# Kernel tuning notes

Measured on AMD Instinct MI355X. Metric: run time of the kernel, lower is better.

## Reference

```python
import jax, jax.numpy as jnp
import numpy as np

N_NODES = 50000
N_EDGES = 800000
IN_DIM = 256
OUT_DIM = 64
NEG_SLOPE = 0.01  # torch F.leaky_relu default


def setup_inputs() -> dict:
    key = jax.random.key(0)
    k1, k2, k3, k4, k5 = jax.random.split(key, 5)
    return {
        "h": jax.random.normal(k1, (N_NODES, IN_DIM), dtype=jnp.float32),
        "src": jax.random.randint(k2, (N_EDGES,), 0, N_NODES, dtype=jnp.int32),
        "dst": jax.random.randint(k3, (N_EDGES,), 0, N_NODES, dtype=jnp.int32),
        "W_fc": jax.random.normal(k4, (IN_DIM, OUT_DIM), dtype=jnp.float32) / np.sqrt(IN_DIM),
        "a_vec": jax.random.normal(k5, (2 * OUT_DIM,), dtype=jnp.float32) / np.sqrt(2 * OUT_DIM),
    }


def reference(h, src, dst, W_fc, a_vec):
    n = h.shape[0]
    d = W_fc.shape[1]
    # z = fc(h)
    z = h @ W_fc  # [N, out_dim]
    # edge attention: attn_fc(cat[z_src, z_dst]) == z_src@a[:d] + z_dst@a[d:]
    s_src = z @ a_vec[:d]  # [N]
    s_dst = z @ a_vec[d:]  # [N]
    e = jax.nn.leaky_relu(s_src[src] + s_dst[dst], negative_slope=NEG_SLOPE)  # [E]
    # segment softmax over incoming edges of each dst node (stable)
    e_max = jax.ops.segment_max(e, dst, num_segments=n)  # -inf for isolated nodes (unused)
    e_exp = jnp.exp(e - e_max[dst])
    denom = jax.ops.segment_sum(e_exp, dst, num_segments=n)
    alpha = e_exp / denom[dst]  # [E]
    # weighted scatter-sum of source features
    out = jax.ops.segment_sum(alpha[:, None] * z[src], dst, num_segments=n)  # [N, out_dim]
    return out
```

## Files before the change

kernel.cpp:

```cpp
#include <hip/hip_runtime.h>

#define IN_DIM 256
#define OUT_DIM 64
#define NEG_SLOPE 0.01f
#define SCAN_CHUNK 2048

__global__ __launch_bounds__(256) void gemm_z(const float* __restrict__ h,
                                              const float* __restrict__ W,
                                              const float* __restrict__ a,
                                              float* __restrict__ z,
                                              float* __restrict__ s_src,
                                              float* __restrict__ s_dst, int n) {
    __shared__ float hT[64][68];
    __shared__ float Wc[64][OUT_DIM];
    const int tid = threadIdx.x;
    const int row0 = blockIdx.x * 64;
    const int tr = tid >> 4;
    const int tc = tid & 15;

    float acc[4][4] = {};

    for (int kc = 0; kc < IN_DIM / 64; ++kc) {
        __syncthreads();
        #pragma unroll
        for (int p = 0; p < 4; ++p) {
            int r  = (tid >> 4) + p * 16;
            int k4 = (tid & 15) * 4;
            int grow = row0 + r;
            float4 hv = make_float4(0.f, 0.f, 0.f, 0.f);
            if (grow < n)
                hv = *(const float4*)&h[(size_t)grow * IN_DIM + kc * 64 + k4];
            hT[k4 + 0][r] = hv.x;
            hT[k4 + 1][r] = hv.y;
            hT[k4 + 2][r] = hv.z;
            hT[k4 + 3][r] = hv.w;
            *(float4*)&Wc[r][k4] =
                *(const float4*)&W[(size_t)(kc * 64 + r) * OUT_DIM + k4];
        }
        __syncthreads();
        #pragma unroll 8
        for (int k = 0; k < 64; ++k) {
            float4 hv = *(const float4*)&hT[k][tr * 4];
            float4 wv = *(const float4*)&Wc[k][tc * 4];
            acc[0][0] = fmaf(hv.x, wv.x, acc[0][0]);
            acc[0][1] = fmaf(hv.x, wv.y, acc[0][1]);
            acc[0][2] = fmaf(hv.x, wv.z, acc[0][2]);
            acc[0][3] = fmaf(hv.x, wv.w, acc[0][3]);
            acc[1][0] = fmaf(hv.y, wv.x, acc[1][0]);
            acc[1][1] = fmaf(hv.y, wv.y, acc[1][1]);
            acc[1][2] = fmaf(hv.y, wv.z, acc[1][2]);
            acc[1][3] = fmaf(hv.y, wv.w, acc[1][3]);
            acc[2][0] = fmaf(hv.z, wv.x, acc[2][0]);
            acc[2][1] = fmaf(hv.z, wv.y, acc[2][1]);
            acc[2][2] = fmaf(hv.z, wv.z, acc[2][2]);
            acc[2][3] = fmaf(hv.z, wv.w, acc[2][3]);
            acc[3][0] = fmaf(hv.w, wv.x, acc[3][0]);
            acc[3][1] = fmaf(hv.w, wv.y, acc[3][1]);
            acc[3][2] = fmaf(hv.w, wv.z, acc[3][2]);
            acc[3][3] = fmaf(hv.w, wv.w, acc[3][3]);
        }
    }

    #pragma unroll
    for (int i = 0; i < 4; ++i) {
        int row = row0 + tr * 4 + i;
        if (row < n) {
            float4 v = make_float4(acc[i][0], acc[i][1], acc[i][2], acc[i][3]);
            *(float4*)&z[(size_t)row * OUT_DIM + tc * 4] = v;
        }
    }

    float a1[4], a2[4];
    #pragma unroll
    for (int j = 0; j < 4; ++j) {
        a1[j] = a[tc * 4 + j];
        a2[j] = a[OUT_DIM + tc * 4 + j];
    }
    #pragma unroll
    for (int i = 0; i < 4; ++i) {
        float p1 = 0.f, p2 = 0.f;
        #pragma unroll
        for (int j = 0; j < 4; ++j) {
            p1 = fmaf(acc[i][j], a1[j], p1);
            p2 = fmaf(acc[i][j], a2[j], p2);
        }
        #pragma unroll
        for (int o = 1; o < 16; o <<= 1) {
            p1 += __shfl_xor(p1, o);
            p2 += __shfl_xor(p2, o);
        }
        int row = row0 + tr * 4 + i;
        if (tc == 0 && row < n) {
            s_src[row] = p1;
            s_dst[row] = p2;
        }
    }
}

__global__ __launch_bounds__(256) void count_deg(const int* __restrict__ dst,
                                                 int* __restrict__ deg,
                                                 int* __restrict__ rank, int E) {
    int i = blockIdx.x * 256 + threadIdx.x;
    if (i >= E) return;
    rank[i] = atomicAdd(&deg[dst[i]], 1);
}

__global__ __launch_bounds__(256) void block_sums(const int* __restrict__ deg,
                                                  int* __restrict__ bsum, int n) {
    __shared__ int red[256];
    const int tid = threadIdx.x;
    int base = blockIdx.x * SCAN_CHUNK + tid * 8;
    int s = 0;
    #pragma unroll
    for (int j = 0; j < 8; ++j)
        if (base + j < n) s += deg[base + j];
    red[tid] = s;
    __syncthreads();
    #pragma unroll
    for (int d = 128; d; d >>= 1) {
        if (tid < d) red[tid] += red[tid + d];
        __syncthreads();
    }
    if (tid == 0) bsum[blockIdx.x] = red[0];
}

__global__ __launch_bounds__(256) void scan_bsums(const int* __restrict__ bsum,
                                                  int* __restrict__ ebase,
                                                  int* __restrict__ off, int nb, int n) {
    __shared__ int ts[256];
    const int tid = threadIdx.x;
    int v = (tid < nb) ? bsum[tid] : 0;
    ts[tid] = v;
    __syncthreads();
    #pragma unroll
    for (int d = 1; d < 256; d <<= 1) {
        int add = (tid >= d) ? ts[tid - d] : 0;
        __syncthreads();
        ts[tid] += add;
        __syncthreads();
    }
    if (tid < nb) ebase[tid] = ts[tid] - v;
    if (tid == 255) off[n] = ts[255];
}

__global__ __launch_bounds__(256) void scan_local(const int* __restrict__ deg,
                                                  const int* __restrict__ ebase,
                                                  int* __restrict__ off, int n) {
    __shared__ int ts[256];
    const int tid = threadIdx.x;
    int base = blockIdx.x * SCAN_CHUNK + tid * 8;
    int v[8];
    int s = 0;
    #pragma unroll
    for (int j = 0; j < 8; ++j) {
        v[j] = (base + j < n) ? deg[base + j] : 0;
        s += v[j];
    }
    ts[tid] = s;
    __syncthreads();
    #pragma unroll
    for (int d = 1; d < 256; d <<= 1) {
        int add = (tid >= d) ? ts[tid - d] : 0;
        __syncthreads();
        ts[tid] += add;
        __syncthreads();
    }
    int run = ebase[blockIdx.x] + ts[tid] - s;
    #pragma unroll
    for (int j = 0; j < 8; ++j) {
        if (base + j < n) off[base + j] = run;
        run += v[j];
    }
}

__global__ __launch_bounds__(256) void scatter_csr(const int* __restrict__ src,
                                                   const int* __restrict__ dst,
                                                   const float* __restrict__ s_src,
                                                   const float* __restrict__ s_dst,
                                                   const int* __restrict__ off,
                                                   const int* __restrict__ rank,
                                                   int2* __restrict__ csr, int E) {
    int i = blockIdx.x * 256 + threadIdx.x;
    if (i >= E) return;
    int s = src[i], t = dst[i];
    float x = s_src[s] + s_dst[t];
    x = x > 0.f ? x : NEG_SLOPE * x;
    float w = __expf(x);
    int pos = off[t] + rank[i];
    csr[pos] = make_int2(s, __float_as_int(w));
}

__global__ __launch_bounds__(256) void aggregate(const int* __restrict__ off,
                                                 const int2* __restrict__ csr,
                                                 const float* __restrict__ z,
                                                 float* __restrict__ out, int n) {
    int node = blockIdx.x * 4 + (threadIdx.x >> 6);
    int lane = threadIdx.x & 63;
    if (node >= n) return;
    int beg = off[node];
    int end = off[node + 1];

    float acc = 0.f;
    float s = 0.f;
    int j = beg;
    for (; j + 3 < end; j += 4) {
        int2 e0 = csr[j];
        int2 e1 = csr[j + 1];
        int2 e2 = csr[j + 2];
        int2 e3 = csr[j + 3];
        float w0 = __int_as_float(e0.y);
        float w1 = __int_as_float(e1.y);
        float w2 = __int_as_float(e2.y);
        float w3 = __int_as_float(e3.y);
        float z0 = z[(size_t)e0.x * OUT_DIM + lane];
        float z1 = z[(size_t)e1.x * OUT_DIM + lane];
        float z2 = z[(size_t)e2.x * OUT_DIM + lane];
        float z3 = z[(size_t)e3.x * OUT_DIM + lane];
        acc = fmaf(w0, z0, acc);
        acc = fmaf(w1, z1, acc);
        acc = fmaf(w2, z2, acc);
        acc = fmaf(w3, z3, acc);
        s += (w0 + w1) + (w2 + w3);
    }
    for (; j < end; ++j) {
        int2 e0 = csr[j];
        float w0 = __int_as_float(e0.y);
        acc = fmaf(w0, z[(size_t)e0.x * OUT_DIM + lane], acc);
        s += w0;
    }
    float inv = (end > beg) ? 1.0f / s : 0.f;
    out[(size_t)node * OUT_DIM + lane] = acc * inv;
}

extern "C" void kernel_launch(void* const* d_in, const int* in_sizes, int n_in,
                              void* d_out, int out_size, void* d_ws, size_t ws_size,
                              hipStream_t stream) {
    const float* h   = (const float*)d_in[0];
    const int*   src = (const int*)d_in[1];
    const int*   dst = (const int*)d_in[2];
    const float* W   = (const float*)d_in[3];
    const float* a   = (const float*)d_in[4];
    float* out = (float*)d_out;

    const int n = in_sizes[0] / IN_DIM;
    const int E = in_sizes[1];
    const int nb = (n + SCAN_CHUNK - 1) / SCAN_CHUNK;

    char* ws = (char*)d_ws;
    size_t off_b = 0;
    auto alloc = [&](size_t bytes) -> void* {
        void* p = ws + off_b;
        off_b += (bytes + 255) & ~(size_t)255;
        return p;
    };
    float* z     = (float*)alloc((size_t)n * OUT_DIM * sizeof(float));
    float* s_src = (float*)alloc((size_t)n * sizeof(float));
    float* s_dst = (float*)alloc((size_t)n * sizeof(float));
    int*   deg   = (int*)alloc((size_t)n * sizeof(int));
    int*   offs  = (int*)alloc((size_t)(n + 1) * sizeof(int));
    int*   rank  = (int*)alloc((size_t)E * sizeof(int));
    int*   bsum  = (int*)alloc(256 * sizeof(int));
    int*   ebase = (int*)alloc(256 * sizeof(int));
    int2*  csr   = (int2*)alloc((size_t)E * sizeof(int2));

    hipMemsetAsync(deg, 0, (size_t)n * sizeof(int), stream);

    gemm_z<<<(n + 63) / 64, 256, 0, stream>>>(h, W, a, z, s_src, s_dst, n);
    count_deg<<<(E + 255) / 256, 256, 0, stream>>>(dst, deg, rank, E);
    block_sums<<<nb, 256, 0, stream>>>(deg, bsum, n);
    scan_bsums<<<1, 256, 0, stream>>>(bsum, ebase, offs, nb, n);
    scan_local<<<nb, 256, 0, stream>>>(deg, ebase, offs, n);
    scatter_csr<<<(E + 255) / 256, 256, 0, stream>>>(src, dst, s_src, s_dst, offs,
                                                     rank, csr, E);
    aggregate<<<(n + 3) / 4, 256, 0, stream>>>(offs, csr, z, out, n);
}
```

Before: 224.3 us.

## Use bf16 MFMA for the feature GEMM and store z in bf16

Replaces the scalar FP32 tiled GEMM with a bf16 MFMA 16x16x32 kernel. h is converted to bf16 in shared memory, and W is pre-transposed to bf16 by a small extra kernel. z is now written as bf16, which halves the bytes the aggregate kernel gathers per edge. The attention scores are still computed from the fp32 accumulators. In exchange, precision drops: z and the GEMM inputs are rounded to bf16, which may affect tolerance, and there is one extra kernel launch.

```diff
diff --git a/kernel.cpp b/kernel.cpp
--- a/kernel.cpp
+++ b/kernel.cpp
@@ -4,95 +4,120 @@
 #define OUT_DIM 64
 #define NEG_SLOPE 0.01f
 #define SCAN_CHUNK 2048
-
-__global__ __launch_bounds__(256) void gemm_z(const float* __restrict__ h,
-                                              const float* __restrict__ W,
-                                              const float* __restrict__ a,
-                                              float* __restrict__ z,
-                                              float* __restrict__ s_src,
-                                              float* __restrict__ s_dst, int n) {
-    __shared__ float hT[64][68];
-    __shared__ float Wc[64][OUT_DIM];
+#define HBS 280
+
+typedef short short8 __attribute__((ext_vector_type(8)));
+typedef float f32x4 __attribute__((ext_vector_type(4)));
+typedef unsigned short u16x4 __attribute__((ext_vector_type(4)));
+typedef unsigned short u16x8 __attribute__((ext_vector_type(8)));
+
+__device__ __forceinline__ unsigned short f2b(float f) {
+    unsigned u = __float_as_uint(f);
+    return (unsigned short)((u + 0x7FFFu + ((u >> 16) & 1u)) >> 16);
+}
+__device__ __forceinline__ float b2f(unsigned short b) {
+    return __uint_as_float(((unsigned)b) << 16);
+}
+
+__global__ __launch_bounds__(256) void w_conv(const float* __restrict__ W,
+                                              unsigned short* __restrict__ Wt) {
+    int g = blockIdx.x * 256 + threadIdx.x;
+    int k = g >> 6, c = g & 63;
+    Wt[c * IN_DIM + k] = f2b(W[k * OUT_DIM + c]);
+}
+
+__global__ __launch_bounds__(256) void gemm_mfma(const float* __restrict__ h,
+                                                 const unsigned short* __restrict__ Wt,
+                                                 const float* __restrict__ a,
+                                                 unsigned short* __restrict__ zb,
+                                                 float* __restrict__ s_src,
+                                                 float* __restrict__ s_dst, int n) {
+    __shared__ unsigned short hb[64 * HBS];
+    __shared__ unsigned short wb[64 * HBS];
+    __shared__ float sp1[2][64];
+    __shared__ float sp2[2][64];
     const int tid = threadIdx.x;
+    const int lane = tid & 63;
+    const int w = tid >> 6;
     const int row0 = blockIdx.x * 64;
-    const int tr = tid >> 4;
-    const int tc = tid & 15;
-
-    float acc[4][4] = {};
-
-    for (int kc = 0; kc < IN_DIM / 64; ++kc) {
-        __syncthreads();
-        #pragma unroll
-        for (int p = 0; p < 4; ++p) {
-            int r  = (tid >> 4) + p * 16;
-            int k4 = (tid & 15) * 4;
-            int grow = row0 + r;
+
+    {
+        int c = tid >> 2, seg = tid & 3;
+        #pragma unroll
+        for (int i = 0; i < 8; ++i) {
+            u16x8 v = *(const u16x8*)&Wt[c * IN_DIM + seg * 64 + i * 8];
+            *(u16x8*)&wb[c * HBS + seg * 64 + i * 8] = v;
+        }
+    }
+    {
+        int r = tid >> 2, seg = tid & 3;
+        int grow = row0 + r;
+        #pragma unroll
+        for (int i = 0; i < 16; ++i) {
             float4 hv = make_float4(0.f, 0.f, 0.f, 0.f);
             if (grow < n)
-                hv = *(const float4*)&h[(size_t)grow * IN_DIM + kc * 64 + k4];
-            hT[k4 + 0][r] = hv.x;
-            hT[k4 + 1][r] = hv.y;
-            hT[k4 + 2][r] = hv.z;
-            hT[k4 + 3][r] = hv.w;
-            *(float4*)&Wc[r][k4] =
-                *(const float4*)&W[(size_t)(kc * 64 + r) * OUT_DIM + k4];
+                hv = *(const float4*)&h[(size_t)grow * IN_DIM + seg * 64 + i * 4];
+            u16x4 p;
+            p[0] = f2b(hv.x); p[1] = f2b(hv.y); p[2] = f2b(hv.z); p[3] = f2b(hv.w);
+            *(u16x4*)&hb[r * HBS + seg * 64 + i * 4] = p;
         }
-        __syncthreads();
-        #pragma unroll 8
-        for (int k = 0; k < 64; ++k) {
-            float4 hv = *(const float4*)&hT[k][tr * 4];
-            float4 wv = *(const float4*)&Wc[k][tc * 4];
-            acc[0][0] = fmaf(hv.x, wv.x, acc[0][0]);
-            acc[0][1] = fmaf(hv.x, wv.y, acc[0][1]);
-            acc[0][2] = fmaf(hv.x, wv.z, acc[0][2]);
-            acc[0][3] = fmaf(hv.x, wv.w, acc[0][3]);
-            acc[1][0] = fmaf(hv.y, wv.x, acc[1][0]);
-            acc[1][1] = fmaf(hv.y, wv.y, acc[1][1]);
-            acc[1][2] = fmaf(hv.y, wv.z, acc[1][2]);
-            acc[1][3] = fmaf(hv.y, wv.w, acc[1][3]);
-            acc[2][0] = fmaf(hv.z, wv.x, acc[2][0]);
-            acc[2][1] = fmaf(hv.z, wv.y, acc[2][1]);
-            acc[2][2] = fmaf(hv.z, wv.z, acc[2][2]);
-            acc[2][3] = fmaf(hv.z, wv.w, acc[2][3]);
-            acc[3][0] = fmaf(hv.w, wv.x, acc[3][0]);
-            acc[3][1] = fmaf(hv.w, wv.y, acc[3][1]);
-            acc[3][2] = fmaf(hv.w, wv.z, acc[3][2]);
-            acc[3][3] = fmaf(hv.w, wv.w, acc[3][3]);
+    }
+    __syncthreads();
+
+    const int rw = (w & 1) * 32;
+    const int cw = (w >> 1) * 32;
+    const int l16 = lane & 15;
+    const int q = lane >> 4;
+
+    f32x4 acc[2][2] = {};
+    #pragma unroll
+    for (int ks = 0; ks < 8; ++ks) {
+        short8 af[2], bf[2];
+        #pragma unroll
+        for (int i = 0; i < 2; ++i)
+            af[i] = *(const short8*)&hb[(rw + i * 16 + l16) * HBS + ks * 32 + q * 8];
+        #pragma unroll
+        for (int j = 0; j < 2; ++j)
+            bf[j] = *(const short8*)&wb[(cw + j * 16 + l16) * HBS + ks * 32 + q * 8];
+        #pragma unroll
+        for (int i = 0; i < 2; ++i)
+            #pragma unroll
+            for (int j = 0; j < 2; ++j)
+                acc[i][j] = __builtin_amdgcn_mfma_f32_16x16x32_bf16(af[i], bf[j], acc[i][j], 0, 0, 0);
+    }
+
+    #pragma unroll
+    for (int i = 0; i < 2; ++i) {
+        #pragma unroll
+        for (int reg = 0; reg < 4; ++reg) {
+            int row_local = rw + i * 16 + q * 4 + reg;
+            int grow = row0 + row_local;
+            float p1 = 0.f, p2 = 0.f;
+            #pragma unroll
+            for (int j = 0; j < 2; ++j) {
+                int col = cw + j * 16 + l16;
+                float zv = acc[i][j][reg];
+                if (grow < n) zb[(size_t)grow * OUT_DIM + col] = f2b(zv);
+                p1 = fmaf(zv, a[col], p1);
+                p2 = fmaf(zv, a[OUT_DIM + col], p2);
+            }
+            #pragma unroll
+            for (int o = 1; o < 16; o <<= 1) {
+                p1 += __shfl_xor(p1, o);
+                p2 += __shfl_xor(p2, o);
+            }
+            if (l16 == 0) {
+                sp1[w >> 1][row_local] = p1;
+                sp2[w >> 1][row_local] = p2;
+            }
         }
     }
-
-    #pragma unroll
-    for (int i = 0; i < 4; ++i) {
-        int row = row0 + tr * 4 + i;
-        if (row < n) {
-            float4 v = make_float4(acc[i][0], acc[i][1], acc[i][2], acc[i][3]);
-            *(float4*)&z[(size_t)row * OUT_DIM + tc * 4] = v;
-        }
-    }
-
-    float a1[4], a2[4];
-    #pragma unroll
-    for (int j = 0; j < 4; ++j) {
-        a1[j] = a[tc * 4 + j];
-        a2[j] = a[OUT_DIM + tc * 4 + j];
-    }
-    #pragma unroll
-    for (int i = 0; i < 4; ++i) {
-        float p1 = 0.f, p2 = 0.f;
-        #pragma unroll
-        for (int j = 0; j < 4; ++j) {
-            p1 = fmaf(acc[i][j], a1[j], p1);
-            p2 = fmaf(acc[i][j], a2[j], p2);
-        }
-        #pragma unroll
-        for (int o = 1; o < 16; o <<= 1) {
-            p1 += __shfl_xor(p1, o);
-            p2 += __shfl_xor(p2, o);
-        }
-        int row = row0 + tr * 4 + i;
-        if (tc == 0 && row < n) {
-            s_src[row] = p1;
-            s_dst[row] = p2;
+    __syncthreads();
+    if (tid < 64) {
+        int grow = row0 + tid;
+        if (grow < n) {
+            s_src[grow] = sp1[0][tid] + sp1[1][tid];
+            s_dst[grow] = sp2[0][tid] + sp2[1][tid];
         }
     }
 }
@@ -192,7 +217,7 @@
 
 __global__ __launch_bounds__(256) void aggregate(const int* __restrict__ off,
                                                  const int2* __restrict__ csr,
-                                                 const float* __restrict__ z,
+                                                 const unsigned short* __restrict__ zb,
                                                  float* __restrict__ out, int n) {
     int node = blockIdx.x * 4 + (threadIdx.x >> 6);
     int lane = threadIdx.x & 63;
@@ -212,10 +237,10 @@
         float w1 = __int_as_float(e1.y);
         float w2 = __int_as_float(e2.y);
         float w3 = __int_as_float(e3.y);
-        float z0 = z[(size_t)e0.x * OUT_DIM + lane];
-        float z1 = z[(size_t)e1.x * OUT_DIM + lane];
-        float z2 = z[(size_t)e2.x * OUT_DIM + lane];
-        float z3 = z[(size_t)e3.x * OUT_DIM + lane];
+        float z0 = b2f(zb[(size_t)e0.x * OUT_DIM + lane]);
+        float z1 = b2f(zb[(size_t)e1.x * OUT_DIM + lane]);
+        float z2 = b2f(zb[(size_t)e2.x * OUT_DIM + lane]);
+        float z3 = b2f(zb[(size_t)e3.x * OUT_DIM + lane]);
         acc = fmaf(w0, z0, acc);
         acc = fmaf(w1, z1, acc);
         acc = fmaf(w2, z2, acc);
@@ -225,7 +250,7 @@
     for (; j < end; ++j) {
         int2 e0 = csr[j];
         float w0 = __int_as_float(e0.y);
-        acc = fmaf(w0, z[(size_t)e0.x * OUT_DIM + lane], acc);
+        acc = fmaf(w0, b2f(zb[(size_t)e0.x * OUT_DIM + lane]), acc);
         s += w0;
     }
     float inv = (end > beg) ? 1.0f / s : 0.f;
@@ -253,24 +278,26 @@
         off_b += (bytes + 255) & ~(size_t)255;
         return p;
     };
-    float* z     = (float*)alloc((size_t)n * OUT_DIM * sizeof(float));
-    float* s_src = (float*)alloc((size_t)n * sizeof(float));
-    float* s_dst = (float*)alloc((size_t)n * sizeof(float));
-    int*   deg   = (int*)alloc((size_t)n * sizeof(int));
-    int*   offs  = (int*)alloc((size_t)(n + 1) * sizeof(int));
-    int*   rank  = (int*)alloc((size_t)E * sizeof(int));
-    int*   bsum  = (int*)alloc(256 * sizeof(int));
-    int*   ebase = (int*)alloc(256 * sizeof(int));
-    int2*  csr   = (int2*)alloc((size_t)E * sizeof(int2));
+    unsigned short* zb   = (unsigned short*)alloc((size_t)n * OUT_DIM * sizeof(unsigned short));
+    unsigned short* Wt   = (unsigned short*)alloc((size_t)IN_DIM * OUT_DIM * sizeof(unsigned short));
+    float*          s_src= (float*)alloc((size_t)n * sizeof(float));
+    float*          s_dst= (float*)alloc((size_t)n * sizeof(float));
+    int*            deg  = (int*)alloc((size_t)n * sizeof(int));
+    int*            offs = (int*)alloc((size_t)(n + 1) * sizeof(int));
+    int*            rank = (int*)alloc((size_t)E * sizeof(int));
+    int*            bsum = (int*)alloc(256 * sizeof(int));
+    int*            ebase= (int*)alloc(256 * sizeof(int));
+    int2*           csr  = (int2*)alloc((size_t)E * sizeof(int2));
 
     hipMemsetAsync(deg, 0, (size_t)n * sizeof(int), stream);
 
-    gemm_z<<<(n + 63) / 64, 256, 0, stream>>>(h, W, a, z, s_src, s_dst, n);
+    w_conv<<<64, 256, 0, stream>>>(W, Wt);
+    gemm_mfma<<<(n + 63) / 64, 256, 0, stream>>>(h, Wt, a, zb, s_src, s_dst, n);
     count_deg<<<(E + 255) / 256, 256, 0, stream>>>(dst, deg, rank, E);
     block_sums<<<nb, 256, 0, stream>>>(deg, bsum, n);
     scan_bsums<<<1, 256, 0, stream>>>(bsum, ebase, offs, nb, n);
     scan_local<<<nb, 256, 0, stream>>>(deg, ebase, offs, n);
     scatter_csr<<<(E + 255) / 256, 256, 0, stream>>>(src, dst, s_src, s_dst, offs,
                                                      rank, csr, E);
-    aggregate<<<(n + 3) / 4, 256, 0, stream>>>(offs, csr, z, out, n);
-}
+    aggregate<<<(n + 3) / 4, 256, 0, stream>>>(offs, csr, zb, out, n);
+}
```

New measurement: 208.6 us. 7.0% less time.
